# Performance work log

Measured on AMD Instinct MI355X. Metric: run time of the kernel, lower is better.

Reference implementation:

```python
import jax, jax.numpy as jnp
import numpy as np

N_NODES = 50000
E_RAW = 1600000
EMB_DIM = 32
HID = 128
OUT = 128


def setup_inputs() -> dict:
    key = jax.random.key(0)
    k1, k2, k3, k4, k5, k6 = jax.random.split(key, 6)
    x = jnp.arange(N_NODES, dtype=jnp.int64)
    edge_index = jax.random.randint(k1, (2, E_RAW), 0, N_NODES, dtype=jnp.int64)
    emb = jax.random.normal(k2, (N_NODES, EMB_DIM), dtype=jnp.float32)
    W1 = jax.random.normal(k3, (EMB_DIM, HID), dtype=jnp.float32) / np.sqrt(EMB_DIM)
    b1 = jnp.zeros((HID,), dtype=jnp.float32)
    W2 = jax.random.normal(k4, (HID, OUT), dtype=jnp.float32) / np.sqrt(HID)
    b2 = jnp.zeros((OUT,), dtype=jnp.float32)
    return {"x": x, "edge_index": edge_index, "emb": emb,
            "W1": W1, "b1": b1, "W2": W2, "b2": b2}


def _gcn_norm(edge_index, num_nodes):
    # add self-loops, then symmetric normalization deg^-1/2 A_hat deg^-1/2
    loop = jnp.arange(num_nodes, dtype=edge_index.dtype)
    src = jnp.concatenate([edge_index[0], loop])
    dst = jnp.concatenate([edge_index[1], loop])
    ones = jnp.ones(src.shape[0], dtype=jnp.float32)
    deg = jax.ops.segment_sum(ones, dst, num_segments=num_nodes)
    dinv = jax.lax.rsqrt(deg)  # deg >= 1 due to self-loops
    norm = dinv[src] * dinv[dst]  # [E+N]
    return src, dst, norm


def _gcn_conv(h, src, dst, norm, W, b, num_nodes):
    h = h @ W                                  # [N, d_out] dense GEMM
    msg = h[src] * norm[:, None]               # gather + edge scale
    agg = jax.ops.segment_sum(msg, dst, num_segments=num_nodes)  # scatter-add
    return agg + b


def reference(x, edge_index, emb, W1, b1, W2, b2):
    num_nodes = emb.shape[0]
    h = emb[x]                                 # embedding lookup
    src, dst, norm = _gcn_norm(edge_index, num_nodes)
    h = _gcn_conv(h, src, dst, norm, W1, b1, num_nodes)
    h = jax.nn.relu(h)
    out = _gcn_conv(h, src, dst, norm, W2, b2, num_nodes)
    return out
```

## Files before the change

kernel.cpp:

```cpp
#include <hip/hip_runtime.h>


#define NPP   6250
#define NC    32

static inline int cdiv(int a, int b){ return (a + b - 1) / b; }

__device__ __forceinline__ unsigned short f2bf(float f){
    unsigned int u = __float_as_uint(f);
    u += 0x7fffu + ((u >> 16) & 1u);
    return (unsigned short)(u >> 16);
}
__device__ __forceinline__ float bf2f(unsigned short b){
    return __uint_as_float(((unsigned int)b) << 16);
}

__global__ void k_zero_i32(int* __restrict__ p, int n){
    int i = blockIdx.x * blockDim.x + threadIdx.x;
    if (i < n) p[i] = 0;
}

__global__ __launch_bounds__(256) void k_bucket(const int* __restrict__ src,
        const int* __restrict__ dst, int E, int* __restrict__ staged_s,
        int* __restrict__ staged_d, int* __restrict__ gcur, int npp, int C){
    __shared__ int  qcnt[8];
    __shared__ int  qbase[8];
    __shared__ int2 qbuf[8 * 256];
    int tid = threadIdx.x;
    if (tid < 8) qcnt[tid] = 0;
    __syncthreads();
    int e0 = blockIdx.x * 1024 + tid * 4;
    if (e0 + 3 < E){
        int4 d4 = *(const int4*)(dst + e0);
        int4 s4 = *(const int4*)(src + e0);
        int dd[4] = {d4.x, d4.y, d4.z, d4.w};
        int ss[4] = {s4.x, s4.y, s4.z, s4.w};
        #pragma unroll
        for (int i = 0; i < 4; i++){
            int p = dd[i] / npp;
            int pos = atomicAdd(&qcnt[p], 1);
            if (pos < 256) qbuf[p * 256 + pos] = make_int2(ss[i], dd[i]);
            else {
                int gp = atomicAdd(&gcur[p], 1);
                staged_s[(size_t)p * C + gp] = ss[i];
                staged_d[(size_t)p * C + gp] = dd[i];
            }
        }
    } else {
        for (int e = e0; e < E && e < e0 + 4; e++){
            int d = dst[e], s = src[e];
            int p = d / npp;
            int pos = atomicAdd(&qcnt[p], 1);
            if (pos < 256) qbuf[p * 256 + pos] = make_int2(s, d);
            else {
                int gp = atomicAdd(&gcur[p], 1);
                staged_s[(size_t)p * C + gp] = s;
                staged_d[(size_t)p * C + gp] = d;
            }
        }
    }
    __syncthreads();
    if (tid < 8){
        int nq = min(qcnt[tid], 256);
        qbase[tid] = (nq > 0) ? atomicAdd(&gcur[tid], nq) : 0;
    }
    __syncthreads();
    for (int b = 0; b < 8; b++){
        int nq = min(qcnt[b], 256);
        int gb = qbase[b];
        for (int i = tid; i < nq; i += 256){
            int2 pr = qbuf[b * 256 + i];
            staged_s[(size_t)b * C + gb + i] = pr.x;
            staged_d[(size_t)b * C + gb + i] = pr.y;
        }
    }
}

__global__ __launch_bounds__(256) void k_hist(const int* __restrict__ staged_d,
        const int* __restrict__ gcur, int C, int CH, int npp, int* __restrict__ H){
    __shared__ int hist[NPP];
    int part  = blockIdx.x & 7;
    int chunk = blockIdx.x >> 3;
    int tid = threadIdx.x;
    for (int i = tid; i < npp; i += 256) hist[i] = 0;
    __syncthreads();
    int pc = gcur[part];
    int lo = part * npp;
    int e0 = chunk * CH, e1 = min(e0 + CH, pc);
    const int* sd = staged_d + (size_t)part * C;
    for (int e = e0 + tid; e < e1; e += 256)
        atomicAdd(&hist[sd[e] - lo], 1);
    __syncthreads();
    int* Hrow = H + (size_t)(part * NC + chunk) * npp;
    for (int i = tid; i < npp; i += 256) Hrow[i] = hist[i];
}

__global__ __launch_bounds__(256) void k_nodescan(int* __restrict__ H, int npp, int n,
        int* __restrict__ ecount, float* __restrict__ dinv, int* __restrict__ bsum){
    __shared__ int s[256];
    int t = blockIdx.x * 256 + threadIdx.x;
    int run = 0;
    if (t < 8 * npp && t < n){
        int p  = t / npp;
        int dl = t - p * npp;
        #pragma unroll
        for (int c = 0; c < NC; c++){
            size_t idx = (size_t)(p * NC + c) * npp + dl;
            int v = H[idx];
            H[idx] = run;
            run += v;
        }
        ecount[t] = run;
        dinv[t] = rsqrtf((float)run + 1.0f);
    }
    s[threadIdx.x] = run;
    __syncthreads();
    for (int d = 128; d > 0; d >>= 1){
        if (threadIdx.x < d) s[threadIdx.x] += s[threadIdx.x + d];
        __syncthreads();
    }
    if (threadIdx.x == 0) bsum[blockIdx.x] = s[0];
}

__global__ __launch_bounds__(256) void k_scanBC(const int* __restrict__ ecount, int n,
        const int* __restrict__ bsum, int nb, int* __restrict__ offsets){
    __shared__ int bs[256];
    __shared__ int s[256];
    int t = threadIdx.x;
    bs[t] = (t < nb) ? bsum[t] : 0;
    __syncthreads();
    if (t == 0){
        int run = 0;
        for (int b = 0; b < nb; b++){ int v = bs[b]; bs[b] = run; run += v; }
    }
    __syncthreads();
    int i = blockIdx.x * 256 + t;
    int v = (i < n) ? ecount[i] : 0;
    s[t] = v;
    __syncthreads();
    for (int d = 1; d < 256; d <<= 1){
        int x = (t >= d) ? s[t - d] : 0;
        __syncthreads();
        s[t] += x;
        __syncthreads();
    }
    if (i < n) offsets[i] = bs[blockIdx.x] + s[t] - v;
}

__global__ __launch_bounds__(256) void k_fill3(const int* __restrict__ staged_s,
        const int* __restrict__ staged_d, const int* __restrict__ gcur, int C, int CH,
        int npp, const int* __restrict__ H, const int* __restrict__ offsets,
        int* __restrict__ csr_src){
    __shared__ int cur[NPP];
    int part  = blockIdx.x & 7;
    int chunk = blockIdx.x >> 3;
    int tid = threadIdx.x;
    const int* Hrow = H + (size_t)(part * NC + chunk) * npp;
    for (int i = tid; i < npp; i += 256) cur[i] = Hrow[i];
    __syncthreads();
    int pc = gcur[part];
    int lo = part * npp;
    int e0 = chunk * CH, e1 = min(e0 + CH, pc);
    const int* ss = staged_s + (size_t)part * C;
    const int* sd = staged_d + (size_t)part * C;
    for (int e = e0 + tid; e < e1; e += 256){
        int d = sd[e];
        int r = atomicAdd(&cur[d - lo], 1);
        csr_src[offsets[d] + r] = ss[e];
    }
}

__global__ void k_scale(const float* __restrict__ emb, const int* __restrict__ x,
                        const float* __restrict__ dinv, unsigned short* __restrict__ es, int n){
    int idx = blockIdx.x * blockDim.x + threadIdx.x;
    if (idx >= n * 32) return;
    int i = idx >> 5;
    int c = idx & 31;
    es[idx] = f2bf(emb[(size_t)x[i] * 32 + c] * dinv[i]);
}

__global__ __launch_bounds__(256) void k_l1(const unsigned short* __restrict__ es,
        const int* __restrict__ offsets, const int* __restrict__ ecount,
        const int* __restrict__ csr, const float* __restrict__ dinv,
        const float* __restrict__ W1, const float* __restrict__ b1,
        unsigned short* __restrict__ hs, int n){
    __shared__ float w[32 * 128];
    __shared__ float a1t[8][32];
    for (int i = threadIdx.x; i < 32 * 128; i += 256) w[i] = W1[i];
    int g    = threadIdx.x >> 5;
    int lane = threadIdx.x & 31;
    int node = blockIdx.x * 8 + g;
    if (node < n){
        int off = offsets[node], cnt = ecount[node];
        float s0 = bf2f(es[(size_t)node * 32 + lane]);
        float s1 = 0.f;
        int e = 0;
        for (; e + 8 <= cnt; e += 8){
            int i0 = csr[off + e + 0], i1 = csr[off + e + 1];
            int i2 = csr[off + e + 2], i3 = csr[off + e + 3];
            int i4 = csr[off + e + 4], i5 = csr[off + e + 5];
            int i6 = csr[off + e + 6], i7 = csr[off + e + 7];
            unsigned short v0 = es[(size_t)i0 * 32 + lane];
            unsigned short v1 = es[(size_t)i1 * 32 + lane];
            unsigned short v2 = es[(size_t)i2 * 32 + lane];
            unsigned short v3 = es[(size_t)i3 * 32 + lane];
            unsigned short v4 = es[(size_t)i4 * 32 + lane];
            unsigned short v5 = es[(size_t)i5 * 32 + lane];
            unsigned short v6 = es[(size_t)i6 * 32 + lane];
            unsigned short v7 = es[(size_t)i7 * 32 + lane];
            s0 += bf2f(v0) + bf2f(v2) + bf2f(v4) + bf2f(v6);
            s1 += bf2f(v1) + bf2f(v3) + bf2f(v5) + bf2f(v7);
        }
        for (; e < cnt; e++) s0 += bf2f(es[(size_t)csr[off + e] * 32 + lane]);
        a1t[g][lane] = dinv[node] * (s0 + s1);
    }
    __syncthreads();
    if (node >= n) return;
    int c4 = lane * 4;
    float4 acc = *(const float4*)(b1 + c4);
    #pragma unroll
    for (int k4 = 0; k4 < 8; k4++){
        float4 av = *(const float4*)&a1t[g][k4 * 4];
        float4 w0 = *(const float4*)&w[(k4 * 4 + 0) * 128 + c4];
        float4 w1 = *(const float4*)&w[(k4 * 4 + 1) * 128 + c4];
        float4 w2 = *(const float4*)&w[(k4 * 4 + 2) * 128 + c4];
        float4 w3 = *(const float4*)&w[(k4 * 4 + 3) * 128 + c4];
        acc.x += av.x * w0.x + av.y * w1.x + av.z * w2.x + av.w * w3.x;
        acc.y += av.x * w0.y + av.y * w1.y + av.z * w2.y + av.w * w3.y;
        acc.z += av.x * w0.z + av.y * w1.z + av.z * w2.z + av.w * w3.z;
        acc.w += av.x * w0.w + av.y * w1.w + av.z * w2.w + av.w * w3.w;
    }
    float dv = dinv[node];
    ushort4 o;
    o.x = f2bf(dv * fmaxf(acc.x, 0.f));
    o.y = f2bf(dv * fmaxf(acc.y, 0.f));
    o.z = f2bf(dv * fmaxf(acc.z, 0.f));
    o.w = f2bf(dv * fmaxf(acc.w, 0.f));
    *(ushort4*)(hs + (size_t)node * 128 + c4) = o;
}

__global__ __launch_bounds__(256) void k_l2(const unsigned short* __restrict__ hs,
        const int* __restrict__ offsets, const int* __restrict__ ecount,
        const int* __restrict__ csr, const float* __restrict__ dinv,
        const float* __restrict__ W2, const float* __restrict__ b2,
        float* __restrict__ out, int n){
    __shared__ float a2t[32 * 128];
    int g    = threadIdx.x >> 5;
    int lane = threadIdx.x & 31;
    int c4g  = lane * 4;
    #pragma unroll
    for (int j = 0; j < 4; j++){
        int nl = g + 8 * j;
        int node = blockIdx.x * 32 + nl;
        if (node < n){
            int off = offsets[node], cnt = ecount[node];
            ushort4 sv = *(const ushort4*)(hs + (size_t)node * 128 + c4g);
            float ax0 = bf2f(sv.x), ax1 = 0.f;
            float ay0 = bf2f(sv.y), ay1 = 0.f;
            float az0 = bf2f(sv.z), az1 = 0.f;
            float aw0 = bf2f(sv.w), aw1 = 0.f;
            int e = 0;
            for (; e + 8 <= cnt; e += 8){
                int i0 = csr[off + e + 0], i1 = csr[off + e + 1];
                int i2 = csr[off + e + 2], i3 = csr[off + e + 3];
                int i4 = csr[off + e + 4], i5 = csr[off + e + 5];
                int i6 = csr[off + e + 6], i7 = csr[off + e + 7];
                ushort4 v0 = *(const ushort4*)(hs + (size_t)i0 * 128 + c4g);
                ushort4 v1 = *(const ushort4*)(hs + (size_t)i1 * 128 + c4g);
                ushort4 v2 = *(const ushort4*)(hs + (size_t)i2 * 128 + c4g);
                ushort4 v3 = *(const ushort4*)(hs + (size_t)i3 * 128 + c4g);
                ushort4 v4 = *(const ushort4*)(hs + (size_t)i4 * 128 + c4g);
                ushort4 v5 = *(const ushort4*)(hs + (size_t)i5 * 128 + c4g);
                ushort4 v6 = *(const ushort4*)(hs + (size_t)i6 * 128 + c4g);
                ushort4 v7 = *(const ushort4*)(hs + (size_t)i7 * 128 + c4g);
                ax0 += bf2f(v0.x) + bf2f(v2.x) + bf2f(v4.x) + bf2f(v6.x);
                ax1 += bf2f(v1.x) + bf2f(v3.x) + bf2f(v5.x) + bf2f(v7.x);
                ay0 += bf2f(v0.y) + bf2f(v2.y) + bf2f(v4.y) + bf2f(v6.y);
                ay1 += bf2f(v1.y) + bf2f(v3.y) + bf2f(v5.y) + bf2f(v7.y);
                az0 += bf2f(v0.z) + bf2f(v2.z) + bf2f(v4.z) + bf2f(v6.z);
                az1 += bf2f(v1.z) + bf2f(v3.z) + bf2f(v5.z) + bf2f(v7.z);
                aw0 += bf2f(v0.w) + bf2f(v2.w) + bf2f(v4.w) + bf2f(v6.w);
                aw1 += bf2f(v1.w) + bf2f(v3.w) + bf2f(v5.w) + bf2f(v7.w);
            }
            for (; e < cnt; e++){
                ushort4 v = *(const ushort4*)(hs + (size_t)csr[off + e] * 128 + c4g);
                ax0 += bf2f(v.x); ay0 += bf2f(v.y); az0 += bf2f(v.z); aw0 += bf2f(v.w);
            }
            float dv = dinv[node];
            float4 r;
            r.x = dv * (ax0 + ax1); r.y = dv * (ay0 + ay1);
            r.z = dv * (az0 + az1); r.w = dv * (aw0 + aw1);
            *(float4*)&a2t[nl * 128 + c4g] = r;
        }
    }
    __syncthreads();
    int c4 = lane * 4;
    int r0 = (threadIdx.x >> 5) * 4;
    float4 bias = *(const float4*)(b2 + c4);
    float4 acc0 = bias, acc1 = bias, acc2 = bias, acc3 = bias;
    for (int k = 0; k < 128; k += 4){
        float4 a0  = *(const float4*)&a2t[(r0 + 0) * 128 + k];
        float4 a1v = *(const float4*)&a2t[(r0 + 1) * 128 + k];
        float4 a2v = *(const float4*)&a2t[(r0 + 2) * 128 + k];
        float4 a3v = *(const float4*)&a2t[(r0 + 3) * 128 + k];
        #pragma unroll
        for (int kk = 0; kk < 4; kk++){
            float4 wv = *(const float4*)(W2 + (size_t)(k + kk) * 128 + c4);
            float b0 = (kk == 0) ? a0.x  : (kk == 1) ? a0.y  : (kk == 2) ? a0.z  : a0.w;
            float b1v= (kk == 0) ? a1v.x : (kk == 1) ? a1v.y : (kk == 2) ? a1v.z : a1v.w;
            float b2v= (kk == 0) ? a2v.x : (kk == 1) ? a2v.y : (kk == 2) ? a2v.z : a2v.w;
            float b3 = (kk == 0) ? a3v.x : (kk == 1) ? a3v.y : (kk == 2) ? a3v.z : a3v.w;
            acc0.x += b0 * wv.x; acc0.y += b0 * wv.y; acc0.z += b0 * wv.z; acc0.w += b0 * wv.w;
            acc1.x += b1v * wv.x; acc1.y += b1v * wv.y; acc1.z += b1v * wv.z; acc1.w += b1v * wv.w;
            acc2.x += b2v * wv.x; acc2.y += b2v * wv.y; acc2.z += b2v * wv.z; acc2.w += b2v * wv.w;
            acc3.x += b3 * wv.x; acc3.y += b3 * wv.y; acc3.z += b3 * wv.z; acc3.w += b3 * wv.w;
        }
    }
    int rb = blockIdx.x * 32 + r0;
    if (rb + 0 < n) *(float4*)(out + (size_t)(rb + 0) * 128 + c4) = acc0;
    if (rb + 1 < n) *(float4*)(out + (size_t)(rb + 1) * 128 + c4) = acc1;
    if (rb + 2 < n) *(float4*)(out + (size_t)(rb + 2) * 128 + c4) = acc2;
    if (rb + 3 < n) *(float4*)(out + (size_t)(rb + 3) * 128 + c4) = acc3;
}

extern "C" void kernel_launch(void* const* d_in, const int* in_sizes, int n_in,
                              void* d_out, int out_size, void* d_ws, size_t ws_size,
                              hipStream_t stream){
    const int*   x    = (const int*)d_in[0];
    const int*   ei   = (const int*)d_in[1];
    const float* emb  = (const float*)d_in[2];
    const float* W1   = (const float*)d_in[3];
    const float* b1   = (const float*)d_in[4];
    const float* W2   = (const float*)d_in[5];
    const float* b2   = (const float*)d_in[6];
    const int N = in_sizes[0];
    const int E = in_sizes[1] / 2;
    const int* srcv = ei;
    const int* dstv = ei + E;
    float* out = (float*)d_out;

    char* p = (char*)d_ws;
    auto alloc = [&](size_t bytes) -> char* {
        char* r = p; p += (bytes + 255) & ~(size_t)255; return r;
    };
    int nb = cdiv(N, 256);
    int*            ecount  = (int*)           alloc((size_t)(N + 8) * 4);
    int*            gcur    = ecount + N;
    int*            offsets = (int*)           alloc((size_t)N * 4);
    int*            bsum    = (int*)           alloc((size_t)nb * 4);
    float*          dinv    = (float*)         alloc((size_t)N * 4);
    int*            csr     = (int*)           alloc((size_t)E * 4);
    unsigned short* es      = (unsigned short*)alloc((size_t)N * 32 * 2);
    int*            H       = (int*)           alloc((size_t)8 * NC * NPP * 4);
    unsigned short* hs      = (unsigned short*)alloc((size_t)N * 128 * 2);
    int*            staged  = (int*)           alloc((size_t)2 * (E + 8 * 65536) * 4);
    (void)ws_size; (void)n_in; (void)out_size;

    const int npp = cdiv(N, 8);
    const int C   = E / 8 + 65536;
    const int CH  = cdiv(C, NC);
    int* staged_s = staged;
    int* staged_d = staged_s + (size_t)8 * C;

    k_zero_i32<<<1, 64, 0, stream>>>(gcur, 8);
    k_bucket  <<<cdiv(E, 1024), 256, 0, stream>>>(srcv, dstv, E, staged_s, staged_d, gcur, npp, C);
    k_hist    <<<8 * NC, 256, 0, stream>>>(staged_d, gcur, C, CH, npp, H);
    k_nodescan<<<nb, 256, 0, stream>>>(H, npp, N, ecount, dinv, bsum);
    k_scanBC  <<<nb, 256, 0, stream>>>(ecount, N, bsum, nb, offsets);
    k_fill3   <<<8 * NC, 256, 0, stream>>>(staged_s, staged_d, gcur, C, CH, npp, H, offsets, csr);

    k_scale <<<cdiv(N * 32, 256), 256, 0, stream>>>(emb, x, dinv, es, N);
    k_l1    <<<cdiv(N, 8), 256, 0, stream>>>(es, offsets, ecount, csr, dinv, W1, b1, hs, N);

    k_l2    <<<cdiv(N, 32), 256, 0, stream>>>(hs, offsets, ecount, csr, dinv, W2, b2, out, N);
}
```

Before: 273.7 us.

## Pack staged edges into one int, vectorize gathers, retile layer-1 GEMM

Staged edges are packed as a single 32-bit word (local dst in the high 15 bits, src in the low 17 bits), halving the staging traffic in bucket, hist and fill. Layer 1 now gathers ushort4 per lane with 8 lanes per node and 32 nodes per block, and its 32x128 transform uses a 4-row register tile. Layer 2 gathers uint4 (8 bf16) per lane with 16 lanes per node. The aim is fewer memory transactions and better reuse of W1 per block. The packing assumes node ids fit in 17 bits and per-partition indices in 15 bits.

```diff
diff --git a/kernel.cpp b/kernel.cpp
--- a/kernel.cpp
+++ b/kernel.cpp
@@ -14,6 +14,8 @@
 __device__ __forceinline__ float bf2f(unsigned short b){
     return __uint_as_float(((unsigned int)b) << 16);
 }
+__device__ __forceinline__ float bflo(unsigned int u){ return __uint_as_float(u << 16); }
+__device__ __forceinline__ float bfhi(unsigned int u){ return __uint_as_float(u & 0xffff0000u); }
 
 __global__ void k_zero_i32(int* __restrict__ p, int n){
     int i = blockIdx.x * blockDim.x + threadIdx.x;
@@ -21,11 +23,11 @@
 }
 
 __global__ __launch_bounds__(256) void k_bucket(const int* __restrict__ src,
-        const int* __restrict__ dst, int E, int* __restrict__ staged_s,
-        int* __restrict__ staged_d, int* __restrict__ gcur, int npp, int C){
-    __shared__ int  qcnt[8];
-    __shared__ int  qbase[8];
-    __shared__ int2 qbuf[8 * 256];
+        const int* __restrict__ dst, int E, int* __restrict__ staged,
+        int* __restrict__ gcur, int npp, int C){
+    __shared__ int qcnt[8];
+    __shared__ int qbase[8];
+    __shared__ int qbuf[8 * 256];
     int tid = threadIdx.x;
     if (tid < 8) qcnt[tid] = 0;
     __syncthreads();
@@ -38,24 +40,24 @@
         #pragma unroll
         for (int i = 0; i < 4; i++){
             int p = dd[i] / npp;
+            int pk = ((dd[i] - p * npp) << 17) | ss[i];
             int pos = atomicAdd(&qcnt[p], 1);
-            if (pos < 256) qbuf[p * 256 + pos] = make_int2(ss[i], dd[i]);
+            if (pos < 256) qbuf[p * 256 + pos] = pk;
             else {
                 int gp = atomicAdd(&gcur[p], 1);
-                staged_s[(size_t)p * C + gp] = ss[i];
-                staged_d[(size_t)p * C + gp] = dd[i];
+                staged[(size_t)p * C + gp] = pk;
             }
         }
     } else {
         for (int e = e0; e < E && e < e0 + 4; e++){
             int d = dst[e], s = src[e];
             int p = d / npp;
+            int pk = ((d - p * npp) << 17) | s;
             int pos = atomicAdd(&qcnt[p], 1);
-            if (pos < 256) qbuf[p * 256 + pos] = make_int2(s, d);
+            if (pos < 256) qbuf[p * 256 + pos] = pk;
             else {
                 int gp = atomicAdd(&gcur[p], 1);
-                staged_s[(size_t)p * C + gp] = s;
-                staged_d[(size_t)p * C + gp] = d;
+                staged[(size_t)p * C + gp] = pk;
             }
         }
     }
@@ -68,15 +70,12 @@
     for (int b = 0; b < 8; b++){
         int nq = min(qcnt[b], 256);
         int gb = qbase[b];
-        for (int i = tid; i < nq; i += 256){
-            int2 pr = qbuf[b * 256 + i];
-            staged_s[(size_t)b * C + gb + i] = pr.x;
-            staged_d[(size_t)b * C + gb + i] = pr.y;
-        }
-    }
-}
-
-__global__ __launch_bounds__(256) void k_hist(const int* __restrict__ staged_d,
+        for (int i = tid; i < nq; i += 256)
+            staged[(size_t)b * C + gb + i] = qbuf[b * 256 + i];
+    }
+}
+
+__global__ __launch_bounds__(256) void k_hist(const int* __restrict__ staged,
         const int* __restrict__ gcur, int C, int CH, int npp, int* __restrict__ H){
     __shared__ int hist[NPP];
     int part  = blockIdx.x & 7;
@@ -85,11 +84,10 @@
     for (int i = tid; i < npp; i += 256) hist[i] = 0;
     __syncthreads();
     int pc = gcur[part];
-    int lo = part * npp;
     int e0 = chunk * CH, e1 = min(e0 + CH, pc);
-    const int* sd = staged_d + (size_t)part * C;
+    const int* sd = staged + (size_t)part * C;
     for (int e = e0 + tid; e < e1; e += 256)
-        atomicAdd(&hist[sd[e] - lo], 1);
+        atomicAdd(&hist[(unsigned)sd[e] >> 17], 1);
     __syncthreads();
     int* Hrow = H + (size_t)(part * NC + chunk) * npp;
     for (int i = tid; i < npp; i += 256) Hrow[i] = hist[i];
@@ -147,9 +145,9 @@
     if (i < n) offsets[i] = bs[blockIdx.x] + s[t] - v;
 }
 
-__global__ __launch_bounds__(256) void k_fill3(const int* __restrict__ staged_s,
-        const int* __restrict__ staged_d, const int* __restrict__ gcur, int C, int CH,
-        int npp, const int* __restrict__ H, const int* __restrict__ offsets,
+__global__ __launch_bounds__(256) void k_fill3(const int* __restrict__ staged,
+        const int* __restrict__ gcur, int C, int CH, int npp,
+        const int* __restrict__ H, const int* __restrict__ offsets,
         int* __restrict__ csr_src){
     __shared__ int cur[NPP];
     int part  = blockIdx.x & 7;
@@ -161,12 +159,12 @@
     int pc = gcur[part];
     int lo = part * npp;
     int e0 = chunk * CH, e1 = min(e0 + CH, pc);
-    const int* ss = staged_s + (size_t)part * C;
-    const int* sd = staged_d + (size_t)part * C;
+    const int* sd = staged + (size_t)part * C;
     for (int e = e0 + tid; e < e1; e += 256){
-        int d = sd[e];
-        int r = atomicAdd(&cur[d - lo], 1);
-        csr_src[offsets[d] + r] = ss[e];
+        int pk = sd[e];
+        int dl = (unsigned)pk >> 17;
+        int r = atomicAdd(&cur[dl], 1);
+        csr_src[offsets[lo + dl] + r] = pk & 0x1FFFF;
     }
 }
 
@@ -185,59 +183,94 @@
         const float* __restrict__ W1, const float* __restrict__ b1,
         unsigned short* __restrict__ hs, int n){
     __shared__ float w[32 * 128];
-    __shared__ float a1t[8][32];
+    __shared__ float a1t[32 * 32];
     for (int i = threadIdx.x; i < 32 * 128; i += 256) w[i] = W1[i];
-    int g    = threadIdx.x >> 5;
-    int lane = threadIdx.x & 31;
-    int node = blockIdx.x * 8 + g;
+    int g    = threadIdx.x >> 3;
+    int lane = threadIdx.x & 7;
+    int node = blockIdx.x * 32 + g;
     if (node < n){
         int off = offsets[node], cnt = ecount[node];
-        float s0 = bf2f(es[(size_t)node * 32 + lane]);
-        float s1 = 0.f;
+        int c4 = lane * 4;
+        ushort4 sv = *(const ushort4*)(es + (size_t)node * 32 + c4);
+        float s0 = bf2f(sv.x), s1 = bf2f(sv.y), s2 = bf2f(sv.z), s3 = bf2f(sv.w);
+        float t0 = 0.f, t1 = 0.f, t2 = 0.f, t3 = 0.f;
         int e = 0;
         for (; e + 8 <= cnt; e += 8){
             int i0 = csr[off + e + 0], i1 = csr[off + e + 1];
             int i2 = csr[off + e + 2], i3 = csr[off + e + 3];
             int i4 = csr[off + e + 4], i5 = csr[off + e + 5];
             int i6 = csr[off + e + 6], i7 = csr[off + e + 7];
-            unsigned short v0 = es[(size_t)i0 * 32 + lane];
-            unsigned short v1 = es[(size_t)i1 * 32 + lane];
-            unsigned short v2 = es[(size_t)i2 * 32 + lane];
-            unsigned short v3 = es[(size_t)i3 * 32 + lane];
-            unsigned short v4 = es[(size_t)i4 * 32 + lane];
-            unsigned short v5 = es[(size_t)i5 * 32 + lane];
-            unsigned short v6 = es[(size_t)i6 * 32 + lane];
-            unsigned short v7 = es[(size_t)i7 * 32 + lane];
-            s0 += bf2f(v0) + bf2f(v2) + bf2f(v4) + bf2f(v6);
-            s1 += bf2f(v1) + bf2f(v3) + bf2f(v5) + bf2f(v7);
-        }
-        for (; e < cnt; e++) s0 += bf2f(es[(size_t)csr[off + e] * 32 + lane]);
-        a1t[g][lane] = dinv[node] * (s0 + s1);
-    }
-    __syncthreads();
-    if (node >= n) return;
-    int c4 = lane * 4;
-    float4 acc = *(const float4*)(b1 + c4);
+            ushort4 v0 = *(const ushort4*)(es + (size_t)i0 * 32 + c4);
+            ushort4 v1 = *(const ushort4*)(es + (size_t)i1 * 32 + c4);
+            ushort4 v2 = *(const ushort4*)(es + (size_t)i2 * 32 + c4);
+            ushort4 v3 = *(const ushort4*)(es + (size_t)i3 * 32 + c4);
+            ushort4 v4 = *(const ushort4*)(es + (size_t)i4 * 32 + c4);
+            ushort4 v5 = *(const ushort4*)(es + (size_t)i5 * 32 + c4);
+            ushort4 v6 = *(const ushort4*)(es + (size_t)i6 * 32 + c4);
+            ushort4 v7 = *(const ushort4*)(es + (size_t)i7 * 32 + c4);
+            s0 += bf2f(v0.x) + bf2f(v2.x) + bf2f(v4.x) + bf2f(v6.x);
+            t0 += bf2f(v1.x) + bf2f(v3.x) + bf2f(v5.x) + bf2f(v7.x);
+            s1 += bf2f(v0.y) + bf2f(v2.y) + bf2f(v4.y) + bf2f(v6.y);
+            t1 += bf2f(v1.y) + bf2f(v3.y) + bf2f(v5.y) + bf2f(v7.y);
+            s2 += bf2f(v0.z) + bf2f(v2.z) + bf2f(v4.z) + bf2f(v6.z);
+            t2 += bf2f(v1.z) + bf2f(v3.z) + bf2f(v5.z) + bf2f(v7.z);
+            s3 += bf2f(v0.w) + bf2f(v2.w) + bf2f(v4.w) + bf2f(v6.w);
+            t3 += bf2f(v1.w) + bf2f(v3.w) + bf2f(v5.w) + bf2f(v7.w);
+        }
+        for (; e < cnt; e++){
+            ushort4 v = *(const ushort4*)(es + (size_t)csr[off + e] * 32 + c4);
+            s0 += bf2f(v.x); s1 += bf2f(v.y); s2 += bf2f(v.z); s3 += bf2f(v.w);
+        }
+        float dv = dinv[node];
+        float4 r;
+        r.x = dv * (s0 + t0); r.y = dv * (s1 + t1);
+        r.z = dv * (s2 + t2); r.w = dv * (s3 + t3);
+        *(float4*)&a1t[g * 32 + c4] = r;
+    }
+    __syncthreads();
+    int c4 = (threadIdx.x & 31) * 4;
+    int r0 = (threadIdx.x >> 5) * 4;
+    float4 bias = *(const float4*)(b1 + c4);
+    float4 acc0 = bias, acc1 = bias, acc2 = bias, acc3 = bias;
+    for (int k = 0; k < 32; k += 4){
+        float4 a0  = *(const float4*)&a1t[(r0 + 0) * 32 + k];
+        float4 a1v = *(const float4*)&a1t[(r0 + 1) * 32 + k];
+        float4 a2v = *(const float4*)&a1t[(r0 + 2) * 32 + k];
+        float4 a3v = *(const float4*)&a1t[(r0 + 3) * 32 + k];
+        #pragma unroll
+        for (int kk = 0; kk < 4; kk++){
+            float4 wv = *(const float4*)&w[(k + kk) * 128 + c4];
+            float b0 = (kk == 0) ? a0.x  : (kk == 1) ? a0.y  : (kk == 2) ? a0.z  : a0.w;
+            float b1v= (kk == 0) ? a1v.x : (kk == 1) ? a1v.y : (kk == 2) ? a1v.z : a1v.w;
+            float b2v= (kk == 0) ? a2v.x : (kk == 1) ? a2v.y : (kk == 2) ? a2v.z : a2v.w;
+            float b3 = (kk == 0) ? a3v.x : (kk == 1) ? a3v.y : (kk == 2) ? a3v.z : a3v.w;
+            acc0.x += b0 * wv.x; acc0.y += b0 * wv.y; acc0.z += b0 * wv.z; acc0.w += b0 * wv.w;
+            acc1.x += b1v * wv.x; acc1.y += b1v * wv.y; acc1.z += b1v * wv.z; acc1.w += b1v * wv.w;
+            acc2.x += b2v * wv.x; acc2.y += b2v * wv.y; acc2.z += b2v * wv.z; acc2.w += b2v * wv.w;
+            acc3.x += b3 * wv.x; acc3.y += b3 * wv.y; acc3.z += b3 * wv.z; acc3.w += b3 * wv.w;
+        }
+    }
+    int rb = blockIdx.x * 32 + r0;
     #pragma unroll
-    for (int k4 = 0; k4 < 8; k4++){
-        float4 av = *(const float4*)&a1t[g][k4 * 4];
-        float4 w0 = *(const float4*)&w[(k4 * 4 + 0) * 128 + c4];
-        float4 w1 = *(const float4*)&w[(k4 * 4 + 1) * 128 + c4];
-        float4 w2 = *(const float4*)&w[(k4 * 4 + 2) * 128 + c4];
-        float4 w3 = *(const float4*)&w[(k4 * 4 + 3) * 128 + c4];
-        acc.x += av.x * w0.x + av.y * w1.x + av.z * w2.x + av.w * w3.x;
-        acc.y += av.x * w0.y + av.y * w1.y + av.z * w2.y + av.w * w3.y;
-        acc.z += av.x * w0.z + av.y * w1.z + av.z * w2.z + av.w * w3.z;
-        acc.w += av.x * w0.w + av.y * w1.w + av.z * w2.w + av.w * w3.w;
-    }
-    float dv = dinv[node];
-    ushort4 o;
-    o.x = f2bf(dv * fmaxf(acc.x, 0.f));
-    o.y = f2bf(dv * fmaxf(acc.y, 0.f));
-    o.z = f2bf(dv * fmaxf(acc.z, 0.f));
-    o.w = f2bf(dv * fmaxf(acc.w, 0.f));
-    *(ushort4*)(hs + (size_t)node * 128 + c4) = o;
-}
+    for (int j = 0; j < 4; j++){
+        int node2 = rb + j;
+        if (node2 < n){
+            float4 a = (j == 0) ? acc0 : (j == 1) ? acc1 : (j == 2) ? acc2 : acc3;
+            float dv = dinv[node2];
+            ushort4 o;
+            o.x = f2bf(dv * fmaxf(a.x, 0.f));
+            o.y = f2bf(dv * fmaxf(a.y, 0.f));
+            o.z = f2bf(dv * fmaxf(a.z, 0.f));
+            o.w = f2bf(dv * fmaxf(a.w, 0.f));
+            *(ushort4*)(hs + (size_t)node2 * 128 + c4) = o;
+        }
+    }
+}
+
+#define ACC8(dst, v) { dst[0] += bflo(v.x); dst[1] += bfhi(v.x);  \
+                       dst[2] += bflo(v.y); dst[3] += bfhi(v.y);  \
+                       dst[4] += bflo(v.z); dst[5] += bfhi(v.z);  \
+                       dst[6] += bflo(v.w); dst[7] += bfhi(v.w); }
 
 __global__ __launch_bounds__(256) void k_l2(const unsigned short* __restrict__ hs,
         const int* __restrict__ offsets, const int* __restrict__ ecount,
@@ -245,56 +278,52 @@
         const float* __restrict__ W2, const float* __restrict__ b2,
         float* __restrict__ out, int n){
     __shared__ float a2t[32 * 128];
-    int g    = threadIdx.x >> 5;
-    int lane = threadIdx.x & 31;
-    int c4g  = lane * 4;
+    int g    = threadIdx.x >> 4;
+    int lane = threadIdx.x & 15;
+    int c8   = lane * 8;
     #pragma unroll
-    for (int j = 0; j < 4; j++){
-        int nl = g + 8 * j;
+    for (int j = 0; j < 2; j++){
+        int nl = g + 16 * j;
         int node = blockIdx.x * 32 + nl;
         if (node < n){
             int off = offsets[node], cnt = ecount[node];
-            ushort4 sv = *(const ushort4*)(hs + (size_t)node * 128 + c4g);
-            float ax0 = bf2f(sv.x), ax1 = 0.f;
-            float ay0 = bf2f(sv.y), ay1 = 0.f;
-            float az0 = bf2f(sv.z), az1 = 0.f;
-            float aw0 = bf2f(sv.w), aw1 = 0.f;
+            uint4 sv = *(const uint4*)(hs + (size_t)node * 128 + c8);
+            float s[8] = {bflo(sv.x), bfhi(sv.x), bflo(sv.y), bfhi(sv.y),
+                          bflo(sv.z), bfhi(sv.z), bflo(sv.w), bfhi(sv.w)};
+            float t[8] = {0.f, 0.f, 0.f, 0.f, 0.f, 0.f, 0.f, 0.f};
             int e = 0;
             for (; e + 8 <= cnt; e += 8){
                 int i0 = csr[off + e + 0], i1 = csr[off + e + 1];
                 int i2 = csr[off + e + 2], i3 = csr[off + e + 3];
                 int i4 = csr[off + e + 4], i5 = csr[off + e + 5];
                 int i6 = csr[off + e + 6], i7 = csr[off + e + 7];
-                ushort4 v0 = *(const ushort4*)(hs + (size_t)i0 * 128 + c4g);
-                ushort4 v1 = *(const ushort4*)(hs + (size_t)i1 * 128 + c4g);
-                ushort4 v2 = *(const ushort4*)(hs + (size_t)i2 * 128 + c4g);
-                ushort4 v3 = *(const ushort4*)(hs + (size_t)i3 * 128 + c4g);
-                ushort4 v4 = *(const ushort4*)(hs + (size_t)i4 * 128 + c4g);
-                ushort4 v5 = *(const ushort4*)(hs + (size_t)i5 * 128 + c4g);
-                ushort4 v6 = *(const ushort4*)(hs + (size_t)i6 * 128 + c4g);
-                ushort4 v7 = *(const ushort4*)(hs + (size_t)i7 * 128 + c4g);
-                ax0 += bf2f(v0.x) + bf2f(v2.x) + bf2f(v4.x) + bf2f(v6.x);
-                ax1 += bf2f(v1.x) + bf2f(v3.x) + bf2f(v5.x) + bf2f(v7.x);
-                ay0 += bf2f(v0.y) + bf2f(v2.y) + bf2f(v4.y) + bf2f(v6.y);
-                ay1 += bf2f(v1.y) + bf2f(v3.y) + bf2f(v5.y) + bf2f(v7.y);
-                az0 += bf2f(v0.z) + bf2f(v2.z) + bf2f(v4.z) + bf2f(v6.z);
-                az1 += bf2f(v1.z) + bf2f(v3.z) + bf2f(v5.z) + bf2f(v7.z);
-                aw0 += bf2f(v0.w) + bf2f(v2.w) + bf2f(v4.w) + bf2f(v6.w);
-                aw1 += bf2f(v1.w) + bf2f(v3.w) + bf2f(v5.w) + bf2f(v7.w);
+                uint4 v0 = *(const uint4*)(hs + (size_t)i0 * 128 + c8);
+                uint4 v1 = *(const uint4*)(hs + (size_t)i1 * 128 + c8);
+                uint4 v2 = *(const uint4*)(hs + (size_t)i2 * 128 + c8);
+                uint4 v3 = *(const uint4*)(hs + (size_t)i3 * 128 + c8);
+                uint4 v4 = *(const uint4*)(hs + (size_t)i4 * 128 + c8);
+                uint4 v5 = *(const uint4*)(hs + (size_t)i5 * 128 + c8);
+                uint4 v6 = *(const uint4*)(hs + (size_t)i6 * 128 + c8);
+                uint4 v7 = *(const uint4*)(hs + (size_t)i7 * 128 + c8);
+                ACC8(s, v0); ACC8(t, v1); ACC8(s, v2); ACC8(t, v3);
+                ACC8(s, v4); ACC8(t, v5); ACC8(s, v6); ACC8(t, v7);
             }
             for (; e < cnt; e++){
-                ushort4 v = *(const ushort4*)(hs + (size_t)csr[off + e] * 128 + c4g);
-                ax0 += bf2f(v.x); ay0 += bf2f(v.y); az0 += bf2f(v.z); aw0 += bf2f(v.w);
+                uint4 v = *(const uint4*)(hs + (size_t)csr[off + e] * 128 + c8);
+                ACC8(s, v);
             }
             float dv = dinv[node];
-            float4 r;
-            r.x = dv * (ax0 + ax1); r.y = dv * (ay0 + ay1);
-            r.z = dv * (az0 + az1); r.w = dv * (aw0 + aw1);
-            *(float4*)&a2t[nl * 128 + c4g] = r;
-        }
-    }
-    __syncthreads();
-    int c4 = lane * 4;
+            float4 r1, r2;
+            r1.x = dv * (s[0] + t[0]); r1.y = dv * (s[1] + t[1]);
+            r1.z = dv * (s[2] + t[2]); r1.w = dv * (s[3] + t[3]);
+            r2.x = dv * (s[4] + t[4]); r2.y = dv * (s[5] + t[5]);
+            r2.z = dv * (s[6] + t[6]); r2.w = dv * (s[7] + t[7]);
+            *(float4*)&a2t[nl * 128 + c8]     = r1;
+            *(float4*)&a2t[nl * 128 + c8 + 4] = r2;
+        }
+    }
+    __syncthreads();
+    int c4 = (threadIdx.x & 31) * 4;
     int r0 = (threadIdx.x >> 5) * 4;
     float4 bias = *(const float4*)(b2 + c4);
     float4 acc0 = bias, acc1 = bias, acc2 = bias, acc3 = bias;
@@ -353,24 +382,22 @@
     unsigned short* es      = (unsigned short*)alloc((size_t)N * 32 * 2);
     int*            H       = (int*)           alloc((size_t)8 * NC * NPP * 4);
     unsigned short* hs      = (unsigned short*)alloc((size_t)N * 128 * 2);
-    int*            staged  = (int*)           alloc((size_t)2 * (E + 8 * 65536) * 4);
+    int*            staged  = (int*)           alloc((size_t)(E + 8 * 65536) * 4);
     (void)ws_size; (void)n_in; (void)out_size;
 
     const int npp = cdiv(N, 8);
     const int C   = E / 8 + 65536;
     const int CH  = cdiv(C, NC);
-    int* staged_s = staged;
-    int* staged_d = staged_s + (size_t)8 * C;
 
     k_zero_i32<<<1, 64, 0, stream>>>(gcur, 8);
-    k_bucket  <<<cdiv(E, 1024), 256, 0, stream>>>(srcv, dstv, E, staged_s, staged_d, gcur, npp, C);
-    k_hist    <<<8 * NC, 256, 0, stream>>>(staged_d, gcur, C, CH, npp, H);
+    k_bucket  <<<cdiv(E, 1024), 256, 0, stream>>>(srcv, dstv, E, staged, gcur, npp, C);
+    k_hist    <<<8 * NC, 256, 0, stream>>>(staged, gcur, C, CH, npp, H);
     k_nodescan<<<nb, 256, 0, stream>>>(H, npp, N, ecount, dinv, bsum);
     k_scanBC  <<<nb, 256, 0, stream>>>(ecount, N, bsum, nb, offsets);
-    k_fill3   <<<8 * NC, 256, 0, stream>>>(staged_s, staged_d, gcur, C, CH, npp, H, offsets, csr);
+    k_fill3   <<<8 * NC, 256, 0, stream>>>(staged, gcur, C, CH, npp, H, offsets, csr);
 
     k_scale <<<cdiv(N * 32, 256), 256, 0, stream>>>(emb, x, dinv, es, N);
-    k_l1    <<<cdiv(N, 8), 256, 0, stream>>>(es, offsets, ecount, csr, dinv, W1, b1, hs, N);
+    k_l1    <<<cdiv(N, 32), 256, 0, stream>>>(es, offsets, ecount, csr, dinv, W1, b1, hs, N);
 
     k_l2    <<<cdiv(N, 32), 256, 0, stream>>>(hs, offsets, ecount, csr, dinv, W2, b2, out, N);
 }
```

Result: slower. 295.3 us (+7.9%).
